# Performance work log

Hardware: AMD Instinct MI355X
Metric: run time of the kernel (lower is better)

## Reference

```python
import jax, jax.numpy as jnp
import numpy as np

B, S, H = 1, 2048, 2048
NH, NKV, HD = 32, 8, 64
RBS, ICS, RBN = 64, 64, 16          # retrieval_block_size, input_chunk_size, retrieval_block_num
RLEN = RBS * RBN                     # 1024 retrieval tokens
KV = RLEN + S                        # 3072 total kv length
START = RLEN                         # INPUT_START_IDX
SCALE = HD ** -0.5
NEG = -1e9


def _document_ids():
    # mirrors get_document_ids
    ids = np.full(KV, -1, np.int32)
    ids[:START] = np.arange(START) // RBS + 1            # retrieval blocks -> 1..RBN
    chunk = np.arange(S) // ICS
    ids[START:] = np.where(chunk == 0, -1, np.minimum(chunk, RBN))
    return ids


def _block_mask():
    # mirrors causal_retrieval_mask_mod, precomputed dense [S, KV]
    ids = _document_ids()
    qpos = np.arange(S) + START
    kv = np.arange(KV)
    causal = (qpos[:, None] >= kv[None, :]) & (kv[None, :] > START)
    doc = (ids[qpos][:, None] == ids[None, :]) & (kv[None, :] < START)
    return jnp.asarray(causal | doc)


_MASK = _block_mask()


def _rotate_half(x):
    h = x.shape[-1] // 2
    return jnp.concatenate([-x[..., h:], x[..., :h]], axis=-1)


def setup_inputs() -> dict:
    key = jax.random.key(0)
    ks = jax.random.split(key, 6)
    inv_freq = 1.0 / (10000.0 ** (np.arange(0, HD, 2, dtype=np.float32) / HD))
    ang = np.arange(S, dtype=np.float32)[:, None] * inv_freq[None, :]   # [S, HD/2]
    emb = np.concatenate([ang, ang], axis=-1)                            # [S, HD]
    cos = jnp.asarray(np.cos(emb))[None].astype(jnp.float32)            # [1, S, HD]
    sin = jnp.asarray(np.sin(emb))[None].astype(jnp.float32)
    return {
        "hidden_states": jax.random.normal(ks[0], (B, S, H), jnp.float32),
        "cos": cos,
        "sin": sin,
        "retrieval_key": jax.random.normal(ks[1], (B, NKV, RLEN, HD), jnp.float32),
        "retrieval_value": jax.random.normal(ks[2], (B, NKV, RLEN, HD), jnp.float32),
        "Wq": jax.random.normal(ks[3], (H, NH * HD), jnp.float32) * 0.02,
        "Wk": jax.random.normal(ks[4], (H, NKV * HD), jnp.float32) * 0.02,
        "Wv": jax.random.normal(ks[5], (H, NKV * HD), jnp.float32) * 0.02,
        "Wo": jax.random.normal(jax.random.fold_in(key, 7), (NH * HD, H), jnp.float32) * 0.02,
    }


def reference(hidden_states, cos, sin, retrieval_key, retrieval_value, Wq, Wk, Wv, Wo):
    # QKV projections -> [B, nheads, S, HD]
    q = (hidden_states @ Wq).reshape(B, S, NH, HD).transpose(0, 2, 1, 3)
    k = (hidden_states @ Wk).reshape(B, S, NKV, HD).transpose(0, 2, 1, 3)
    v = (hidden_states @ Wv).reshape(B, S, NKV, HD).transpose(0, 2, 1, 3)
    # RoPE (retrieval kv is pre-encoded; rope only on current tokens)
    c, s = cos[:, None, :, :], sin[:, None, :, :]
    q = q * c + _rotate_half(q) * s
    k = k * c + _rotate_half(k) * s
    # prepend retrieval kv
    k = jnp.concatenate([retrieval_key, k], axis=2)    # [B, NKV, KV, HD]
    v = jnp.concatenate([retrieval_value, v], axis=2)
    # GQA: expand kv heads
    g = NH // NKV
    k = jnp.repeat(k, g, axis=1)                        # [B, NH, KV, HD]
    v = jnp.repeat(v, g, axis=1)
    scores = jnp.einsum("bhqd,bhkd->bhqk", q, k) * SCALE
    scores = jnp.where(_MASK[None, None], scores, NEG)
    probs = jax.nn.softmax(scores, axis=-1)
    # fully-masked rows (q_idx 0) -> zero output, matching flex_attention
    row_valid = _MASK.any(axis=-1)[None, None, :, None]
    probs = jnp.where(row_valid, probs, 0.0)
    out = jnp.einsum("bhqk,bhkd->bhqd", probs, v)
    out = out.transpose(0, 2, 1, 3).reshape(B, S, NH * HD)
    return out @ Wo
```

## Files before the change

kernel.cpp:

```cpp
#include <hip/hip_runtime.h>

#define S_LEN 2048
#define H_DIM 2048
#define NH 32
#define NKV 8
#define HD 64
#define RLEN 1024
#define KVTOT 3072
#define SCALE 0.125f
#define QS 0.18033688011112042f
#define FIX8 11.541560327111707f

typedef unsigned short ushort_t;
using short8 = __attribute__((ext_vector_type(8))) short;
using f32x4 = __attribute__((ext_vector_type(4))) float;

__device__ __forceinline__ float b2f(unsigned short u) {
    union { unsigned int i; float f; } v;
    v.i = ((unsigned int)u) << 16;
    return v.f;
}
__device__ __forceinline__ unsigned short f2b(float f) {
    union { float f; unsigned int i; } v;
    v.f = f;
    unsigned int x = v.i;
    return (unsigned short)((x + 0x7fffu + ((x >> 16) & 1u)) >> 16);
}

__global__ void detect9(const void* p0, const void* p1, const void* p2,
                        const void* p3, const void* p4, const void* p5,
                        const void* p6, const void* p7, const void* p8,
                        int* flags)
{
    __shared__ int bad;
    if (threadIdx.x == 0) bad = 0;
    __syncthreads();
    const void* ps[9] = {p0, p1, p2, p3, p4, p5, p6, p7, p8};
    const unsigned int* w = (const unsigned int*)ps[blockIdx.x];
    int cnt = 0;
    for (int i = threadIdx.x; i < 4096; i += blockDim.x) {
        unsigned int lo = w[i] & 0xFFFFu;
        unsigned int e = (lo >> 7) & 0xFFu;
        if (lo != 0u && (e < 90u || e > 140u)) ++cnt;
    }
    atomicAdd(&bad, cnt);
    __syncthreads();
    if (threadIdx.x == 0) flags[blockIdx.x] = (bad > 16) ? 1 : 0;
}

__global__ void cvt_b(const void* __restrict__ src, ushort_t* __restrict__ dst,
                      int n, const int* __restrict__ F_)
{
    const int F = *F_;
    int i = (blockIdx.x * 256 + threadIdx.x) * 8;
    if (i >= n) return;
    ushort_t o[8];
    if (F) {
        const float* p = (const float*)src + i;
        float4 f0 = ((const float4*)p)[0];
        float4 f1 = ((const float4*)p)[1];
        o[0] = f2b(f0.x); o[1] = f2b(f0.y); o[2] = f2b(f0.z); o[3] = f2b(f0.w);
        o[4] = f2b(f1.x); o[5] = f2b(f1.y); o[6] = f2b(f1.z); o[7] = f2b(f1.w);
        *(uint4*)(dst + i) = *(const uint4*)o;
    } else {
        *(uint4*)(dst + i) = *(const uint4*)((const ushort_t*)src + i);
    }
}

__global__ __launch_bounds__(256) void cvtW(
    const void* __restrict__ Wq, const void* __restrict__ Wk,
    const void* __restrict__ Wv, const void* __restrict__ Wo,
    ushort_t* __restrict__ WqkvT, ushort_t* __restrict__ WoT,
    const int* __restrict__ flags)
{
    const int z = blockIdx.z;
    if ((z == 1 || z == 2) && blockIdx.x >= 8) return;
    const void* src = (z == 0) ? Wq : (z == 1) ? Wk : (z == 2) ? Wv : Wo;
    const int F = flags[5 + z];
    const int C = (z == 1 || z == 2) ? 512 : 2048;
    ushort_t* dst = (z == 3) ? WoT : WqkvT;
    const int rofs = (z == 1) ? 2048 : (z == 2) ? 2560 : 0;

    __shared__ ushort_t S[64 * 72];
    const int r0 = blockIdx.y * 64, c0 = blockIdx.x * 64;
    const int lr = threadIdx.x >> 2, lc = (threadIdx.x & 3) * 16;
    ushort_t t[16];
    if (F) {
        const float* p = (const float*)src + (size_t)(r0 + lr) * C + c0 + lc;
#pragma unroll
        for (int j = 0; j < 16; j += 4) {
            float4 f = *(const float4*)(p + j);
            t[j] = f2b(f.x); t[j + 1] = f2b(f.y); t[j + 2] = f2b(f.z); t[j + 3] = f2b(f.w);
        }
    } else {
        const ushort_t* p = (const ushort_t*)src + (size_t)(r0 + lr) * C + c0 + lc;
        *(uint4*)t = ((const uint4*)p)[0];
        *(uint4*)(t + 8) = ((const uint4*)p)[1];
    }
    *(uint4*)&S[lr * 72 + lc] = *(const uint4*)t;
    *(uint4*)&S[lr * 72 + lc + 8] = *(const uint4*)(t + 8);
    __syncthreads();
    const int wc = threadIdx.x >> 2, wr = (threadIdx.x & 3) * 16;
    ushort_t o[16];
#pragma unroll
    for (int j = 0; j < 16; ++j) o[j] = S[(wr + j) * 72 + wc];
    ushort_t* q = dst + (size_t)(rofs + c0 + wc) * 2048 + r0 + wr;
    *(uint4*)q = *(const uint4*)o;
    *(uint4*)(q + 8) = *(const uint4*)(o + 8);
}

__global__ __launch_bounds__(256) void gemm_qkv(
    const ushort_t* __restrict__ A, const ushort_t* __restrict__ Bt,
    ushort_t* __restrict__ C, int N, int K)
{
    __shared__ __align__(16) ushort_t As[2][64 * 40];
    __shared__ __align__(16) ushort_t Bs[2][128 * 40];
    const int tid = threadIdx.x;
    const int wave = tid >> 6, lane = tid & 63;
    const int lq = lane & 15, quad = lane >> 4;
    const int m0 = blockIdx.y * 64, n0 = blockIdx.x * 128;
    const int wm = (wave & 1) * 32, wn = (wave >> 1) * 64;
    const int ar = tid >> 2, ak = (tid & 3) * 8;
    const int br = tid >> 1, bk = (tid & 1) * 16;
    const int nk = K >> 5;

    f32x4 acc[2][4];
#pragma unroll
    for (int i = 0; i < 2; ++i)
#pragma unroll
        for (int j = 0; j < 4; ++j) acc[i][j] = (f32x4){0.f, 0.f, 0.f, 0.f};

    const ushort_t* ap = A + (size_t)(m0 + ar) * K + ak;
    const ushort_t* bp = Bt + (size_t)(n0 + br) * K + bk;
    {
        uint4 a0 = ((const uint4*)ap)[0];
        uint4 b0 = ((const uint4*)bp)[0], b1 = ((const uint4*)bp)[1];
        *(uint4*)&As[0][ar * 40 + ak] = a0;
        *(uint4*)&Bs[0][br * 40 + bk] = b0; *(uint4*)&Bs[0][br * 40 + bk + 8] = b1;
    }

    for (int kt = 0; kt < nk; ++kt) {
        const int cur = kt & 1;
        uint4 na0, nb0, nb1;
        const bool more = (kt + 1 < nk);
        if (more) {
            na0 = *(const uint4*)(ap + (kt + 1) * 32);
            const ushort_t* bp2 = bp + (kt + 1) * 32;
            nb0 = ((const uint4*)bp2)[0]; nb1 = ((const uint4*)bp2)[1];
        }
        __syncthreads();
        short8 afr[2], bfr[4];
#pragma unroll
        for (int i = 0; i < 2; ++i)
            afr[i] = *(const short8*)&As[cur][(wm + i * 16 + lq) * 40 + quad * 8];
#pragma unroll
        for (int j = 0; j < 4; ++j)
            bfr[j] = *(const short8*)&Bs[cur][(wn + j * 16 + lq) * 40 + quad * 8];
#pragma unroll
        for (int i = 0; i < 2; ++i)
#pragma unroll
            for (int j = 0; j < 4; ++j)
                acc[i][j] = __builtin_amdgcn_mfma_f32_16x16x32_bf16(afr[i], bfr[j], acc[i][j], 0, 0, 0);
        __syncthreads();
        if (more) {
            const int nxt = cur ^ 1;
            *(uint4*)&As[nxt][ar * 40 + ak] = na0;
            *(uint4*)&Bs[nxt][br * 40 + bk] = nb0; *(uint4*)&Bs[nxt][br * 40 + bk + 8] = nb1;
        }
    }

#pragma unroll
    for (int i = 0; i < 2; ++i)
#pragma unroll
        for (int r = 0; r < 4; ++r) {
            ushort_t* cp = C + (size_t)(m0 + wm + i * 16 + quad * 4 + r) * N + n0 + wn + lq;
#pragma unroll
            for (int j = 0; j < 4; ++j) cp[j * 16] = f2b(acc[i][j][r]);
        }
}

__global__ __launch_bounds__(256) void gemm_fin(
    const ushort_t* __restrict__ A, const ushort_t* __restrict__ Bt,
    void* __restrict__ Cv, int N, int K, const int* __restrict__ oF_)
{
    const int oF = *oF_;
    __shared__ __align__(16) ushort_t As[2][64 * 40];
    __shared__ __align__(16) ushort_t Bs[2][128 * 40];
    const int tid = threadIdx.x;
    const int wave = tid >> 6, lane = tid & 63;
    const int lq = lane & 15, quad = lane >> 4;
    const int m0 = blockIdx.y * 64, n0 = blockIdx.x * 128;
    const int wm = (wave & 1) * 32, wn = (wave >> 1) * 64;
    const int ar = tid >> 2, ak = (tid & 3) * 8;
    const int br = tid >> 1, bk = (tid & 1) * 16;
    const int nk = K >> 5;

    f32x4 acc[2][4];
#pragma unroll
    for (int i = 0; i < 2; ++i)
#pragma unroll
        for (int j = 0; j < 4; ++j) acc[i][j] = (f32x4){0.f, 0.f, 0.f, 0.f};

    const ushort_t* ap = A + (size_t)(m0 + ar) * K + ak;
    const ushort_t* bp = Bt + (size_t)(n0 + br) * K + bk;
    {
        uint4 a0 = ((const uint4*)ap)[0];
        uint4 b0 = ((const uint4*)bp)[0], b1 = ((const uint4*)bp)[1];
        *(uint4*)&As[0][ar * 40 + ak] = a0;
        *(uint4*)&Bs[0][br * 40 + bk] = b0; *(uint4*)&Bs[0][br * 40 + bk + 8] = b1;
    }

    for (int kt = 0; kt < nk; ++kt) {
        const int cur = kt & 1;
        uint4 na0, nb0, nb1;
        const bool more = (kt + 1 < nk);
        if (more) {
            na0 = *(const uint4*)(ap + (kt + 1) * 32);
            const ushort_t* bp2 = bp + (kt + 1) * 32;
            nb0 = ((const uint4*)bp2)[0]; nb1 = ((const uint4*)bp2)[1];
        }
        __syncthreads();
        short8 afr[2], bfr[4];
#pragma unroll
        for (int i = 0; i < 2; ++i)
            afr[i] = *(const short8*)&As[cur][(wm + i * 16 + lq) * 40 + quad * 8];
#pragma unroll
        for (int j = 0; j < 4; ++j)
            bfr[j] = *(const short8*)&Bs[cur][(wn + j * 16 + lq) * 40 + quad * 8];
#pragma unroll
        for (int i = 0; i < 2; ++i)
#pragma unroll
            for (int j = 0; j < 4; ++j)
                acc[i][j] = __builtin_amdgcn_mfma_f32_16x16x32_bf16(afr[i], bfr[j], acc[i][j], 0, 0, 0);
        __syncthreads();
        if (more) {
            const int nxt = cur ^ 1;
            *(uint4*)&As[nxt][ar * 40 + ak] = na0;
            *(uint4*)&Bs[nxt][br * 40 + bk] = nb0; *(uint4*)&Bs[nxt][br * 40 + bk + 8] = nb1;
        }
    }

#pragma unroll
    for (int i = 0; i < 2; ++i)
#pragma unroll
        for (int r = 0; r < 4; ++r) {
            size_t off = (size_t)(m0 + wm + i * 16 + quad * 4 + r) * N + n0 + wn + lq;
            if (oF) {
                float* cp = (float*)Cv + off;
#pragma unroll
                for (int j = 0; j < 4; ++j) cp[j * 16] = acc[i][j][r];
            } else {
                ushort_t* cp = (ushort_t*)Cv + off;
#pragma unroll
                for (int j = 0; j < 4; ++j) cp[j * 16] = f2b(acc[i][j][r]);
            }
        }
}

__global__ __launch_bounds__(256) void prepKV(
    const void* __restrict__ rk, const void* __restrict__ rv,
    const ushort_t* __restrict__ qkvp,
    const void* __restrict__ cosv, const void* __restrict__ sinv,
    ushort_t* __restrict__ ktall, ushort_t* __restrict__ vtall,
    const int* __restrict__ flags)
{
    if (blockIdx.z == 0) {
        const int vF = flags[4];
        const int t = blockIdx.x;
        const int kvh = blockIdx.y;
        __shared__ ushort_t S[64 * 72];
        const int lr = threadIdx.x >> 2, lc = (threadIdx.x & 3) * 16;
        ushort_t tt[16];
        if (t < 16) {
            size_t base = ((size_t)kvh * RLEN + t * 64 + lr) * HD + lc;
            if (vF) {
                const float* p = (const float*)rv + base;
#pragma unroll
                for (int j = 0; j < 16; j += 4) {
                    float4 f = *(const float4*)(p + j);
                    tt[j] = f2b(f.x); tt[j + 1] = f2b(f.y); tt[j + 2] = f2b(f.z); tt[j + 3] = f2b(f.w);
                }
            } else {
                const ushort_t* p = (const ushort_t*)rv + base;
                *(uint4*)tt = ((const uint4*)p)[0];
                *(uint4*)(tt + 8) = ((const uint4*)p)[1];
            }
        } else {
            const ushort_t* p = qkvp + (size_t)((t - 16) * 64 + lr) * 3072 + 2560 + kvh * HD + lc;
            *(uint4*)tt = ((const uint4*)p)[0];
            *(uint4*)(tt + 8) = ((const uint4*)p)[1];
        }
        *(uint4*)&S[lr * 72 + lc] = *(const uint4*)tt;
        *(uint4*)&S[lr * 72 + lc + 8] = *(const uint4*)(tt + 8);
        __syncthreads();
        const int wc = threadIdx.x >> 2, wr = (threadIdx.x & 3) * 16;
        ushort_t o[16];
#pragma unroll
        for (int j = 0; j < 16; ++j) o[j] = S[(wr + j) * 72 + wc];
        const int blk = t * 2 + (wr >> 5);
        ushort_t* q = vtall + (((size_t)(kvh * 96 + blk) * 64 + wc) * 32) + (wr & 31);
        *(uint4*)q = *(const uint4*)o;
        *(uint4*)(q + 8) = *(const uint4*)(o + 8);
    } else {
        const int kF = flags[3], cF = flags[1], sF = flags[2];
        int flat = (blockIdx.y * 48 + blockIdx.x) * 256 + threadIdx.x;
        const int d0 = (flat & 3) * 8;
        const int p = (flat >> 2) % KVTOT;
        const int kvh = (flat >> 2) / KVTOT;
        ushort_t o0[8], o1[8];
        if (p < RLEN) {
            size_t base = ((size_t)kvh * RLEN + p) * HD;
            if (kF) {
                const float* s = (const float*)rk + base;
#pragma unroll
                for (int j = 0; j < 8; j += 4) {
                    float4 f = *(const float4*)(s + d0 + j);
                    o0[j] = f2b(f.x); o0[j + 1] = f2b(f.y); o0[j + 2] = f2b(f.z); o0[j + 3] = f2b(f.w);
                    float4 g = *(const float4*)(s + d0 + 32 + j);
                    o1[j] = f2b(g.x); o1[j + 1] = f2b(g.y); o1[j + 2] = f2b(g.z); o1[j + 3] = f2b(g.w);
                }
            } else {
                const ushort_t* s = (const ushort_t*)rk + base;
                *(uint4*)o0 = *(const uint4*)(s + d0);
                *(uint4*)o1 = *(const uint4*)(s + d0 + 32);
            }
        } else {
            const int si = p - RLEN;
            const ushort_t* s = qkvp + (size_t)si * 3072 + 2048 + kvh * HD;
            uint4 u0 = *(const uint4*)(s + d0);
            uint4 u1 = *(const uint4*)(s + d0 + 32);
            const ushort_t* a16 = (const ushort_t*)&u0;
            const ushort_t* b16 = (const ushort_t*)&u1;
            int ci = si * HD + d0;
            float c0[8], c1[8], s0[8], s1[8];
            if (cF) {
                const float* cp = (const float*)cosv + ci;
#pragma unroll
                for (int j = 0; j < 8; ++j) { c0[j] = cp[j]; c1[j] = cp[j + 32]; }
            } else {
                const ushort_t* cp = (const ushort_t*)cosv + ci;
#pragma unroll
                for (int j = 0; j < 8; ++j) { c0[j] = b2f(cp[j]); c1[j] = b2f(cp[j + 32]); }
            }
            if (sF) {
                const float* sp = (const float*)sinv + ci;
#pragma unroll
                for (int j = 0; j < 8; ++j) { s0[j] = sp[j]; s1[j] = sp[j + 32]; }
            } else {
                const ushort_t* sp = (const ushort_t*)sinv + ci;
#pragma unroll
                for (int j = 0; j < 8; ++j) { s0[j] = b2f(sp[j]); s1[j] = b2f(sp[j + 32]); }
            }
#pragma unroll
            for (int j = 0; j < 8; ++j) {
                float a = b2f(a16[j]), b = b2f(b16[j]);
                o0[j] = f2b(a * c0[j] - b * s0[j]);
                o1[j] = f2b(b * c1[j] + a * s1[j]);
            }
        }
        ushort_t* q = ktall + ((size_t)kvh * KVTOT + p) * HD;
        *(uint4*)(q + d0) = *(const uint4*)o0;
        *(uint4*)(q + d0 + 32) = *(const uint4*)o1;
    }
}

__global__ __launch_bounds__(256) void fattn(
    const ushort_t* __restrict__ qkvp, const ushort_t* __restrict__ ktall,
    const ushort_t* __restrict__ vtall, ushort_t* __restrict__ attno,
    const void* __restrict__ cosv, const void* __restrict__ sinv,
    const int* __restrict__ flags)
{
    const int cF = flags[1], sF = flags[2];
    const int h = blockIdx.x;
    const int qb = 31 - blockIdx.y;
    const int kvh = h >> 2;
    const int tid = threadIdx.x;
    const int wave = tid >> 6;
    const int lane = tid & 63;
    const int lq = lane & 15;
    const int quad = lane >> 4;
    const int rb64 = ((qb < 17 ? qb : 16) - 1) * 64;

    __shared__ __align__(16) ushort_t Ks[128 * 72];
    __shared__ __align__(16) ushort_t Ps[4 * 16 * 136];
    ushort_t* pw = &Ps[wave * 16 * 136];

    short8 qfrag[2];
    {
        const int row_g = qb * 64 + wave * 16 + lq;
        const ushort_t* qrow = qkvp + (size_t)row_g * 3072 + h * HD;
        short8 t0 = *(const short8*)(qrow + quad * 8);
        short8 t1 = *(const short8*)(qrow + 32 + quad * 8);
        const int ci = row_g * HD + quad * 8;
        float c0[8], c1[8], s0[8], s1[8];
        if (cF) {
            const float* cp = (const float*)cosv + ci;
#pragma unroll
            for (int j = 0; j < 8; ++j) { c0[j] = cp[j]; c1[j] = cp[j + 32]; }
        } else {
            const ushort_t* cp = (const ushort_t*)cosv + ci;
#pragma unroll
            for (int j = 0; j < 8; ++j) { c0[j] = b2f(cp[j]); c1[j] = b2f(cp[j + 32]); }
        }
        if (sF) {
            const float* sp = (const float*)sinv + ci;
#pragma unroll
            for (int j = 0; j < 8; ++j) { s0[j] = sp[j]; s1[j] = sp[j + 32]; }
        } else {
            const ushort_t* sp = (const ushort_t*)sinv + ci;
#pragma unroll
            for (int j = 0; j < 8; ++j) { s0[j] = b2f(sp[j]); s1[j] = b2f(sp[j + 32]); }
        }
#pragma unroll
        for (int j = 0; j < 8; ++j) {
            float a = b2f((unsigned short)t0[j]), b = b2f((unsigned short)t1[j]);
            qfrag[0][j] = (short)f2b((a * c0[j] - b * s0[j]) * QS);
            qfrag[1][j] = (short)f2b((b * c1[j] + a * s1[j]) * QS);
        }
    }

    f32x4 oacc[4];
#pragma unroll
    for (int nt = 0; nt < 4; ++nt) oacc[nt] = (f32x4){0.f, 0.f, 0.f, 0.f};
    float lsum[4] = {0.f, 0.f, 0.f, 0.f};

    const int Lq = (qb > 0) ? qb * 64 + 128 : 64;
    const int nch = (Lq + 127) >> 7;
    const ushort_t* kbase = ktall + (size_t)kvh * KVTOT * HD;
    const ushort_t* vbase = vtall + (size_t)kvh * 96 * 2048;

    for (int c = 0; c < nch; ++c) {
        uint4 kreg0, kreg1, kreg2, kreg3;
        const int krow = tid >> 1;
        const int kd0 = (tid & 1) * 32;
        {
            int p = c * 128 + krow;
            uint4 z = {0, 0, 0, 0};
            kreg0 = z; kreg1 = z; kreg2 = z; kreg3 = z;
            if (p < Lq) {
                int pk = (qb > 0) ? ((p < 64) ? rb64 + p : 960 + p) : RLEN + p;
                const uint4* s = (const uint4*)(kbase + (size_t)pk * HD + kd0);
                kreg0 = s[0]; kreg1 = s[1]; kreg2 = s[2]; kreg3 = s[3];
            }
        }
        int vblk[4];
#pragma unroll
        for (int kc = 0; kc < 4; ++kc) {
            int p = c * 128 + kc * 32;
            int pk = (qb > 0) ? ((p < 64) ? rb64 + p : 960 + p) : RLEN + p;
            if (pk > KVTOT - 1) pk = KVTOT - 1;
            vblk[kc] = pk >> 5;
        }
        short8 vfA[4], vfB[4];
#pragma unroll
        for (int ntd = 0; ntd < 4; ++ntd)
            vfA[ntd] = *(const short8*)(vbase + ((size_t)vblk[0] * 64 + ntd * 16 + lq) * 32 + quad * 8);
#pragma unroll
        for (int ntd = 0; ntd < 4; ++ntd)
            vfB[ntd] = *(const short8*)(vbase + ((size_t)vblk[1] * 64 + ntd * 16 + lq) * 32 + quad * 8);

        {
            uint4* dk = (uint4*)&Ks[krow * 72 + kd0];
            dk[0] = kreg0; dk[1] = kreg1; dk[2] = kreg2; dk[3] = kreg3;
        }
        __syncthreads();

        const bool lastc = (c == nch - 1) || (qb == 0);
#pragma unroll
        for (int nt = 0; nt < 8; ++nt) {
            f32x4 a = (f32x4){0.f, 0.f, 0.f, 0.f};
            a = __builtin_amdgcn_mfma_f32_16x16x32_bf16(qfrag[0],
                *(const short8*)&Ks[(nt * 16 + lq) * 72 + quad * 8], a, 0, 0, 0);
            a = __builtin_amdgcn_mfma_f32_16x16x32_bf16(qfrag[1],
                *(const short8*)&Ks[(nt * 16 + lq) * 72 + 32 + quad * 8], a, 0, 0, 0);
            const int p = c * 128 + nt * 16 + lq;
#pragma unroll
            for (int r = 0; r < 4; ++r) {
                float pexp = exp2f(a[r] - FIX8);
                if (lastc) {
                    const int qg = qb * 64 + wave * 16 + quad * 4 + r;
                    bool valid;
                    if (qb > 0) valid = (p < 64) || ((p - 64) >= 1 && (p - 64) <= qg);
                    else        valid = (p >= 1 && p <= qg);
                    if (!valid) pexp = 0.f;
                } else if (c == 0) {
                    if (p == 64) pexp = 0.f;
                }
                lsum[r] += pexp;
                pw[(quad * 4 + r) * 136 + nt * 16 + lq] = f2b(pexp);
            }
        }

#pragma unroll
        for (int kc = 0; kc < 4; ++kc) {
            short8 pa = *(const short8*)&pw[lq * 136 + kc * 32 + quad * 8];
            short8 vf0, vf1, vf2, vf3;
            if (kc == 0)      { vf0 = vfA[0]; vf1 = vfA[1]; vf2 = vfA[2]; vf3 = vfA[3]; }
            else if (kc == 1) { vf0 = vfB[0]; vf1 = vfB[1]; vf2 = vfB[2]; vf3 = vfB[3]; }
            else {
                const int b = vblk[kc];
                vf0 = *(const short8*)(vbase + ((size_t)b * 64 + 0 * 16 + lq) * 32 + quad * 8);
                vf1 = *(const short8*)(vbase + ((size_t)b * 64 + 1 * 16 + lq) * 32 + quad * 8);
                vf2 = *(const short8*)(vbase + ((size_t)b * 64 + 2 * 16 + lq) * 32 + quad * 8);
                vf3 = *(const short8*)(vbase + ((size_t)b * 64 + 3 * 16 + lq) * 32 + quad * 8);
            }
            oacc[0] = __builtin_amdgcn_mfma_f32_16x16x32_bf16(pa, vf0, oacc[0], 0, 0, 0);
            oacc[1] = __builtin_amdgcn_mfma_f32_16x16x32_bf16(pa, vf1, oacc[1], 0, 0, 0);
            oacc[2] = __builtin_amdgcn_mfma_f32_16x16x32_bf16(pa, vf2, oacc[2], 0, 0, 0);
            oacc[3] = __builtin_amdgcn_mfma_f32_16x16x32_bf16(pa, vf3, oacc[3], 0, 0, 0);
        }
        __syncthreads();
    }

#pragma unroll
    for (int r = 0; r < 4; ++r) {
        float v = lsum[r];
        v += __shfl_xor(v, 1, 64); v += __shfl_xor(v, 2, 64);
        v += __shfl_xor(v, 4, 64); v += __shfl_xor(v, 8, 64);
        lsum[r] = v;
    }
#pragma unroll
    for (int r = 0; r < 4; ++r) {
        const int qg = qb * 64 + wave * 16 + quad * 4 + r;
        const float inv = (qg == 0) ? 0.f : 1.f / lsum[r];
        ushort_t* orow = attno + (size_t)qg * 2048 + h * HD;
#pragma unroll
        for (int nt = 0; nt < 4; ++nt)
            orow[nt * 16 + lq] = f2b(oacc[nt][r] * inv);
    }
}

extern "C" void kernel_launch(void* const* d_in, const int* in_sizes, int n_in,
                              void* d_out, int out_size, void* d_ws, size_t ws_size,
                              hipStream_t stream) {
    const void* hs   = d_in[0];
    const void* cosv = d_in[1];
    const void* sinv = d_in[2];
    const void* rk   = d_in[3];
    const void* rv   = d_in[4];
    const void* Wq   = d_in[5];
    const void* Wk   = d_in[6];
    const void* Wv   = d_in[7];
    const void* Wo   = d_in[8];

    char* ws = (char*)d_ws;
    int*      flags  = (int*)ws;
    ushort_t* hsb    = (ushort_t*)(ws + (1u  << 20));
    ushort_t* ktall  = hsb;
    ushort_t* vtall  = (ushort_t*)(ws + (1u << 20) + (13u << 18));
    ushort_t* WqkvT  = (ushort_t*)(ws + (9u  << 20));
    ushort_t* attno  = WqkvT;
    ushort_t* WoT    = (ushort_t*)(ws + (21u << 20));
    ushort_t* qkvp   = (ushort_t*)(ws + (29u << 20));

    detect9<<<9, 256, 0, stream>>>(hs, cosv, sinv, rk, rv, Wq, Wk, Wv, Wo, flags);

    cvt_b<<<(H_DIM * S_LEN / 8 + 255) / 256, 256, 0, stream>>>(hs, hsb, H_DIM * S_LEN, flags + 0);
    cvtW<<<dim3(32, 32, 4), 256, 0, stream>>>(Wq, Wk, Wv, Wo, WqkvT, WoT, flags);

    gemm_qkv<<<dim3(3072 / 128, 2048 / 64), 256, 0, stream>>>(hsb, WqkvT, qkvp, 3072, 2048);

    prepKV<<<dim3(48, 8, 2), 256, 0, stream>>>(rk, rv, qkvp, cosv, sinv, ktall, vtall, flags);

    fattn<<<dim3(NH, 32), 256, 0, stream>>>(qkvp, ktall, vtall, attno, cosv, sinv, flags);

    gemm_fin<<<dim3(2048 / 128, 2048 / 64), 256, 0, stream>>>(attno, WoT, d_out, 2048, 2048, flags + 0);
}
```

Measured before the change: 272.2 us.

## Transpose QK MFMA to write packed P rows and reorder query-block schedule

The QK^T MFMA operands are swapped so each lane holds four consecutive key positions for one query row. The probabilities can then be packed with v_cvt_pk_bf16_f32 and written to shared memory as one 8-byte store instead of four scalar 2-byte stores. Row sums collapse to a single per-lane accumulator, reduced across quads and redistributed with shuffles. The grid's query-block order is also changed to interleave heavy and light blocks, aiming for better load balance across CUs at the cost of a bit more index arithmetic.

After: 268.3 us. Within noise of the previous version (-1.4%).

```diff
diff --git a/kernel.cpp b/kernel.cpp
--- a/kernel.cpp
+++ b/kernel.cpp
@@ -372,7 +372,10 @@
 {
     const int cF = flags[1], sF = flags[2];
     const int h = blockIdx.x;
-    const int qb = 31 - blockIdx.y;
+    const int yy = blockIdx.y;
+    const int st = yy >> 3, r8 = yy & 7;
+    const int qb = (st == 0) ? (31 - r8) : (st == 1) ? (16 + r8)
+                 : (st == 2) ? (15 - r8) : r8;
     const int kvh = h >> 2;
     const int tid = threadIdx.x;
     const int wave = tid >> 6;
@@ -380,6 +383,7 @@
     const int lq = lane & 15;
     const int quad = lane >> 4;
     const int rb64 = ((qb < 17 ? qb : 16) - 1) * 64;
+    const int qrow = qb * 64 + wave * 16 + lq;
 
     __shared__ __align__(16) ushort_t Ks[128 * 72];
     __shared__ __align__(16) ushort_t Ps[4 * 16 * 136];
@@ -388,9 +392,9 @@
     short8 qfrag[2];
     {
         const int row_g = qb * 64 + wave * 16 + lq;
-        const ushort_t* qrow = qkvp + (size_t)row_g * 3072 + h * HD;
-        short8 t0 = *(const short8*)(qrow + quad * 8);
-        short8 t1 = *(const short8*)(qrow + 32 + quad * 8);
+        const ushort_t* qrp = qkvp + (size_t)row_g * 3072 + h * HD;
+        short8 t0 = *(const short8*)(qrp + quad * 8);
+        short8 t1 = *(const short8*)(qrp + 32 + quad * 8);
         const int ci = row_g * HD + quad * 8;
         float c0[8], c1[8], s0[8], s1[8];
         if (cF) {
@@ -422,7 +426,7 @@
     f32x4 oacc[4];
 #pragma unroll
     for (int nt = 0; nt < 4; ++nt) oacc[nt] = (f32x4){0.f, 0.f, 0.f, 0.f};
-    float lsum[4] = {0.f, 0.f, 0.f, 0.f};
+    float lsum = 0.f;
 
     const int Lq = (qb > 0) ? qb * 64 + 128 : 64;
     const int nch = (Lq + 127) >> 7;
@@ -469,26 +473,30 @@
 #pragma unroll
         for (int nt = 0; nt < 8; ++nt) {
             f32x4 a = (f32x4){0.f, 0.f, 0.f, 0.f};
-            a = __builtin_amdgcn_mfma_f32_16x16x32_bf16(qfrag[0],
-                *(const short8*)&Ks[(nt * 16 + lq) * 72 + quad * 8], a, 0, 0, 0);
-            a = __builtin_amdgcn_mfma_f32_16x16x32_bf16(qfrag[1],
-                *(const short8*)&Ks[(nt * 16 + lq) * 72 + 32 + quad * 8], a, 0, 0, 0);
-            const int p = c * 128 + nt * 16 + lq;
-#pragma unroll
-            for (int r = 0; r < 4; ++r) {
-                float pexp = exp2f(a[r] - FIX8);
+            a = __builtin_amdgcn_mfma_f32_16x16x32_bf16(
+                *(const short8*)&Ks[(nt * 16 + lq) * 72 + quad * 8], qfrag[0], a, 0, 0, 0);
+            a = __builtin_amdgcn_mfma_f32_16x16x32_bf16(
+                *(const short8*)&Ks[(nt * 16 + lq) * 72 + 32 + quad * 8], qfrag[1], a, 0, 0, 0);
+            float pex[4];
+#pragma unroll
+            for (int rr = 0; rr < 4; ++rr) {
+                const int p = c * 128 + nt * 16 + quad * 4 + rr;
+                float pexp = exp2f(a[rr] - FIX8);
                 if (lastc) {
-                    const int qg = qb * 64 + wave * 16 + quad * 4 + r;
                     bool valid;
-                    if (qb > 0) valid = (p < 64) || ((p - 64) >= 1 && (p - 64) <= qg);
-                    else        valid = (p >= 1 && p <= qg);
+                    if (qb > 0) valid = (p < 64) || ((p - 64) >= 1 && (p - 64) <= qrow);
+                    else        valid = (p >= 1 && p <= qrow);
                     if (!valid) pexp = 0.f;
                 } else if (c == 0) {
                     if (p == 64) pexp = 0.f;
                 }
-                lsum[r] += pexp;
-                pw[(quad * 4 + r) * 136 + nt * 16 + lq] = f2b(pexp);
-            }
+                lsum += pexp;
+                pex[rr] = pexp;
+            }
+            unsigned int w0, w1;
+            asm("v_cvt_pk_bf16_f32 %0, %1, %2" : "=v"(w0) : "v"(pex[0]), "v"(pex[1]));
+            asm("v_cvt_pk_bf16_f32 %0, %1, %2" : "=v"(w1) : "v"(pex[2]), "v"(pex[3]));
+            *(uint2*)&pw[lq * 136 + nt * 16 + quad * 4] = make_uint2(w0, w1);
         }
 
 #pragma unroll
@@ -512,21 +520,18 @@
         __syncthreads();
     }
 
-#pragma unroll
-    for (int r = 0; r < 4; ++r) {
-        float v = lsum[r];
-        v += __shfl_xor(v, 1, 64); v += __shfl_xor(v, 2, 64);
-        v += __shfl_xor(v, 4, 64); v += __shfl_xor(v, 8, 64);
-        lsum[r] = v;
-    }
-#pragma unroll
-    for (int r = 0; r < 4; ++r) {
-        const int qg = qb * 64 + wave * 16 + quad * 4 + r;
-        const float inv = (qg == 0) ? 0.f : 1.f / lsum[r];
+    float tot = lsum;
+    tot += __shfl_xor(tot, 16, 64);
+    tot += __shfl_xor(tot, 32, 64);
+#pragma unroll
+    for (int rr = 0; rr < 4; ++rr) {
+        const int qg = qb * 64 + wave * 16 + quad * 4 + rr;
+        const float tr = __shfl(tot, quad * 4 + rr, 64);
+        const float inv = (qg == 0) ? 0.f : 1.f / tr;
         ushort_t* orow = attno + (size_t)qg * 2048 + h * HD;
 #pragma unroll
         for (int nt = 0; nt < 4; ++nt)
-            orow[nt * 16 + lq] = f2b(oacc[nt][r] * inv);
+            orow[nt * 16 + lq] = f2b(oacc[nt][rr] * inv);
     }
 }
 
```
